# Performance work log

Measured on AMD Instinct MI355X. Metric: run time of the kernel, lower is better.

Reference implementation:

```python
import jax, jax.numpy as jnp
import numpy as np

D_MODEL = 1024
N_REG = 8
D_REG = 32
LN_EPS = 1e-5


def setup_inputs() -> dict:
    key = jax.random.key(0)
    ks = jax.random.split(key, 14)
    s = 0.02
    return {
        "x": jax.random.normal(ks[0], (8, 2048, D_MODEL), dtype=jnp.float32),
        "ln_w": jnp.ones((D_MODEL,), jnp.float32),
        "ln_b": jnp.zeros((D_MODEL,), jnp.float32),
        "Wrq": jax.random.normal(ks[1], (N_REG, D_MODEL), jnp.float32) * s,
        "brq": jax.random.normal(ks[2], (N_REG,), jnp.float32) * s,
        "Wrp": jax.random.normal(ks[3], (D_MODEL, D_REG), jnp.float32) * s,
        "brp": jax.random.normal(ks[4], (D_MODEL,), jnp.float32) * s,
        "Wwq": jax.random.normal(ks[5], (N_REG, D_MODEL), jnp.float32) * s,
        "bwq": jax.random.normal(ks[6], (N_REG,), jnp.float32) * s,
        "Wwv": jax.random.normal(ks[7], (D_REG, D_MODEL), jnp.float32) * s,
        "bwv": jax.random.normal(ks[8], (D_REG,), jnp.float32) * s,
        "Wwg": jax.random.normal(ks[9], (1, D_MODEL), jnp.float32) * s,
        "bwg": jnp.full((1,), -3.0, jnp.float32),
        "mix": jnp.asarray(0.001, jnp.float32),
    }


def _layernorm(x, w, b):
    mu = jnp.mean(x, axis=-1, keepdims=True)
    var = jnp.mean(jnp.square(x - mu), axis=-1, keepdims=True)
    return (x - mu) * jax.lax.rsqrt(var + LN_EPS) * w + b


def _forward(x, ln_w, ln_b, Wrq, brq, Wrp, brp, Wwq, bwq, Wwv, bwv, Wwg, bwg, mix):
    B, L, D = x.shape
    h = _layernorm(x, ln_w, ln_b)  # (B,L,D)
    # Precompute all per-timestep projections as big GEMMs (same math as per-step Linear)
    r_w = jax.nn.softmax(jnp.einsum("bld,rd->blr", h, Wrq) + brq, axis=-1)  # (B,L,R)
    w_w = jax.nn.softmax(jnp.einsum("bld,rd->blr", h, Wwq) + bwq, axis=-1)  # (B,L,R)
    w_v = jnp.einsum("bld,kd->blk", h, Wwv) + bwv                           # (B,L,Dr)
    w_g = jax.nn.sigmoid(jnp.einsum("bld,od->blo", h, Wwg) + bwg)           # (B,L,1)

    def step(registers, inputs):
        rw_t, ww_t, wv_t, wg_t = inputs  # (B,R), (B,R), (B,Dr), (B,1)
        r_v = jnp.einsum("br,brd->bd", rw_t, registers)  # read (B,Dr)
        us = (ww_t * wg_t)[..., None]                     # (B,R,1)
        new_regs = (1.0 - us) * registers + us * wv_t[:, None, :]
        return new_regs, r_v

    init_regs = jnp.zeros((B, N_REG, D_REG), x.dtype)
    seq = (
        jnp.moveaxis(r_w, 1, 0),
        jnp.moveaxis(w_w, 1, 0),
        jnp.moveaxis(w_v, 1, 0),
        jnp.moveaxis(w_g, 1, 0),
    )
    _, r_vs = jax.lax.scan(step, init_regs, seq)  # (L,B,Dr)
    r_vs = jnp.moveaxis(r_vs, 0, 1)               # (B,L,Dr)
    r_out = jnp.einsum("blk,dk->bld", r_vs, Wrp) + brp  # read_proj
    return mix * r_out


def reference(x, ln_w, ln_b, Wrq, brq, Wrp, brp, Wwq, bwq, Wwv, bwv, Wwg, bwg, mix):
    return _forward(x, ln_w, ln_b, Wrq, brq, Wrp, brp, Wwq, bwq, Wwv, bwv, Wwg, bwg, mix)
```

## Files before the change

### kernel.cpp

```cpp
#include <hip/hip_runtime.h>

#define D_MODEL 1024
#define L_SEQ   2048
#define N_BATCH 8
#define N_TOK   (N_BATCH * L_SEQ)
#define N_REGS  8
#define D_REG   32
#define N_CHUNK 64
#define CHUNK   32
#define LN_EPS  1e-5f

#define KC      32
#define XSTR    65
#define XQ      (KC * XSTR)
#define SSTR    57

__device__ __forceinline__ float wred(float v) {
    #pragma unroll
    for (int off = 32; off > 0; off >>= 1) v += __shfl_xor(v, off, 64);
    return v;
}

__device__ __forceinline__ float sigmoidf(float z) {
    return 1.f / (1.f + expf(-z));
}

__global__ __launch_bounds__(256) void k_prep(
    const float* __restrict__ ln_w, const float* __restrict__ ln_b,
    const float* __restrict__ Wrq,  const float* __restrict__ brq,
    const float* __restrict__ Wwq,  const float* __restrict__ bwq,
    const float* __restrict__ Wwv,  const float* __restrict__ bwv,
    const float* __restrict__ Wwg,  const float* __restrict__ bwg,
    float* __restrict__ Wpp, float* __restrict__ c1, float* __restrict__ c2)
{
    const int f = blockIdx.x;
    const int g = f / 13, i = f % 13;

    const float* wrow = nullptr; float bias = 0.f;
    if (f < 8)        { wrow = Wrq + f * D_MODEL;        bias = brq[f]; }
    else if (f < 16)  { wrow = Wwq + (f - 8) * D_MODEL;  bias = bwq[f - 8]; }
    else if (f == 16) { wrow = Wwg;                      bias = bwg[0]; }
    else if (f < 49)  { wrow = Wwv + (f - 17) * D_MODEL; bias = bwv[f - 17]; }

    float p1 = 0.f, p2 = 0.f;
    #pragma unroll
    for (int j = 0; j < 4; ++j) {
        const int k = j * 256 + threadIdx.x;
        float w  = wrow ? wrow[k] : 0.f;
        float wg = w * ln_w[k];
        Wpp[((size_t)(g * D_MODEL + k)) * 16 + i] = wg;
        p1 += wg;
        p2 = fmaf(w, ln_b[k], p2);
    }
    p1 = wred(p1); p2 = wred(p2);

    __shared__ float r1[4], r2[4];
    const int l = threadIdx.x & 63, w = threadIdx.x >> 6;
    if (l == 0) { r1[w] = p1; r2[w] = p2; }
    __syncthreads();
    if (threadIdx.x == 0) {
        c1[f] = r1[0] + r1[1] + r1[2] + r1[3];
        c2[f] = r2[0] + r2[1] + r2[2] + r2[3] + bias;
    }
}

template<int STATS>
__device__ __forceinline__ void proj_chunk(
    const float* __restrict__ lx,
    const float4* __restrict__ wr0,
    int lane, float acc[13], float& st)
{
    #pragma unroll 4
    for (int k = 0; k < KC; ++k) {
        const float xs = lx[k * XSTR + lane];
        const float4* wr = wr0 + (k << 2);
        float4 wa = wr[0], wb = wr[1], wc = wr[2];
        float  wd = reinterpret_cast<const float*>(wr)[12];
        acc[0]  = fmaf(xs, wa.x, acc[0]);
        acc[1]  = fmaf(xs, wa.y, acc[1]);
        acc[2]  = fmaf(xs, wa.z, acc[2]);
        acc[3]  = fmaf(xs, wa.w, acc[3]);
        acc[4]  = fmaf(xs, wb.x, acc[4]);
        acc[5]  = fmaf(xs, wb.y, acc[5]);
        acc[6]  = fmaf(xs, wb.z, acc[6]);
        acc[7]  = fmaf(xs, wb.w, acc[7]);
        acc[8]  = fmaf(xs, wc.x, acc[8]);
        acc[9]  = fmaf(xs, wc.y, acc[9]);
        acc[10] = fmaf(xs, wc.z, acc[10]);
        acc[11] = fmaf(xs, wc.w, acc[11]);
        acc[12] = fmaf(xs, wd,   acc[12]);
        if (STATS == 1) st += xs;
        if (STATS == 2) st = fmaf(xs, xs, st);
    }
}

__global__ __launch_bounds__(1024) void k_lnproj3(
    const float* __restrict__ x,
    const float* __restrict__ Wpp,
    const float* __restrict__ c1, const float* __restrict__ c2,
    float* __restrict__ rw_o, float* __restrict__ us_o, float* __restrict__ wv_o)
{
    extern __shared__ float lds[];
    float* Sb = lds + 2 * 4 * XQ;

    const int tid  = threadIdx.x;
    const int lane = tid & 63;
    const int wv   = tid >> 6;
    const int g    = wv & 3;
    const int kh   = wv >> 2;
    const int tok0 = blockIdx.x * 64;

    const int gs  = __builtin_amdgcn_readfirstlane(g);
    const int khs = __builtin_amdgcn_readfirstlane(kh);

    const int tq  = tid & 255;
    const int row = tq >> 3;
    const int c4  = tq & 7;

    const float4* x4 = reinterpret_cast<const float4*>(x);

    float4 xg[2];
    float acc[13];
    #pragma unroll
    for (int i = 0; i < 13; ++i) acc[i] = 0.f;
    float st = 0.f;

    const size_t gbase = (size_t)(tok0 + row) * 256 + khs * 64 + c4;

    {
        xg[0] = x4[gbase];
        xg[1] = x4[gbase + 32 * 256];
        float* dst = lds + khs * XQ + (c4 * 4) * XSTR;
        #pragma unroll
        for (int p = 0; p < 2; ++p) {
            const int r = row + 32 * p;
            dst[0 * XSTR + r] = xg[p].x;
            dst[1 * XSTR + r] = xg[p].y;
            dst[2 * XSTR + r] = xg[p].z;
            dst[3 * XSTR + r] = xg[p].w;
        }
    }
    __syncthreads();

    for (int c = 0; c < 8; ++c) {
        if (c < 7)  {
            xg[0] = x4[gbase + (size_t)(c + 1) * 8];
            xg[1] = x4[gbase + (size_t)(c + 1) * 8 + 32 * 256];
        }

        const float*  lx  = lds + ((c & 1) * 4 + khs) * XQ;
        const float4* wr0 = reinterpret_cast<const float4*>(Wpp)
                          + ((gs * D_MODEL + khs * 256 + c * KC) << 2);
        if (gs == 1)      proj_chunk<1>(lx, wr0, lane, acc, st);
        else if (gs == 2) proj_chunk<2>(lx, wr0, lane, acc, st);
        else              proj_chunk<0>(lx, wr0, lane, acc, st);

        if (c < 7) {
            float* dst = lds + (((c + 1) & 1) * 4 + khs) * XQ + (c4 * 4) * XSTR;
            #pragma unroll
            for (int p = 0; p < 2; ++p) {
                const int r = row + 32 * p;
                dst[0 * XSTR + r] = xg[p].x;
                dst[1 * XSTR + r] = xg[p].y;
                dst[2 * XSTR + r] = xg[p].z;
                dst[3 * XSTR + r] = xg[p].w;
            }
        }
        __syncthreads();
    }

    if (kh == 0) {
        #pragma unroll
        for (int i = 0; i < 13; ++i) Sb[lane * SSTR + g * 13 + i] = acc[i];
        if (g == 1) Sb[lane * SSTR + 52] = st;
        if (g == 2) Sb[lane * SSTR + 53] = st;
    }
    __syncthreads();
    #pragma unroll
    for (int ph = 1; ph < 4; ++ph) {
        if (kh == ph) {
            #pragma unroll
            for (int i = 0; i < 13; ++i) Sb[lane * SSTR + g * 13 + i] += acc[i];
            if (g == 1) Sb[lane * SSTR + 52] += st;
            if (g == 2) Sb[lane * SSTR + 53] += st;
        }
        __syncthreads();
    }

    if (tid < 256) {
        const int t  = tid & 63;
        const int q  = tid >> 6;
        const int tg = blockIdx.x * 64 + t;
        const float* St = Sb + t * SSTR;

        const float tsum = St[52], tss = St[53];
        const float mu  = tsum * (1.f / D_MODEL);
        const float var = tss * (1.f / D_MODEL) - mu * mu;
        const float rs  = rsqrtf(var + LN_EPS);

        if (q == 0) {
            float lg[8];
            #pragma unroll
            for (int r = 0; r < 8; ++r)
                lg[r] = rs * (St[r] - mu * c1[r]) + c2[r];
            float m = lg[0];
            #pragma unroll
            for (int r = 1; r < 8; ++r) m = fmaxf(m, lg[r]);
            float sm = 0.f;
            #pragma unroll
            for (int r = 0; r < 8; ++r) { lg[r] = expf(lg[r] - m); sm += lg[r]; }
            float inv = 1.f / sm;
            float4* o = reinterpret_cast<float4*>(rw_o + (size_t)tg * 8);
            o[0] = make_float4(lg[0]*inv, lg[1]*inv, lg[2]*inv, lg[3]*inv);
            o[1] = make_float4(lg[4]*inv, lg[5]*inv, lg[6]*inv, lg[7]*inv);
        } else if (q == 1) {
            float lg[8];
            #pragma unroll
            for (int r = 0; r < 8; ++r)
                lg[r] = rs * (St[8 + r] - mu * c1[8 + r]) + c2[8 + r];
            float gl = rs * (St[16] - mu * c1[16]) + c2[16];
            float m = lg[0];
            #pragma unroll
            for (int r = 1; r < 8; ++r) m = fmaxf(m, lg[r]);
            float sm = 0.f;
            #pragma unroll
            for (int r = 0; r < 8; ++r) { lg[r] = expf(lg[r] - m); sm += lg[r]; }
            float inv = sigmoidf(gl) / sm;
            float4* o = reinterpret_cast<float4*>(us_o + (size_t)tg * 8);
            o[0] = make_float4(lg[0]*inv, lg[1]*inv, lg[2]*inv, lg[3]*inv);
            o[1] = make_float4(lg[4]*inv, lg[5]*inv, lg[6]*inv, lg[7]*inv);
        } else {
            const int f0 = 17 + (q - 2) * 16;
            float4* o = reinterpret_cast<float4*>(wv_o + (size_t)tg * 32 + (q - 2) * 16);
            #pragma unroll
            for (int jq = 0; jq < 4; ++jq) {
                float v0 = rs * (St[f0 + jq*4 + 0] - mu * c1[f0 + jq*4 + 0]) + c2[f0 + jq*4 + 0];
                float v1 = rs * (St[f0 + jq*4 + 1] - mu * c1[f0 + jq*4 + 1]) + c2[f0 + jq*4 + 1];
                float v2 = rs * (St[f0 + jq*4 + 2] - mu * c1[f0 + jq*4 + 2]) + c2[f0 + jq*4 + 2];
                float v3 = rs * (St[f0 + jq*4 + 3] - mu * c1[f0 + jq*4 + 3]) + c2[f0 + jq*4 + 3];
                o[jq] = make_float4(v0, v1, v2, v3);
            }
        }
    }
}

__global__ __launch_bounds__(256) void k_chunk(
    const float* __restrict__ us, const float* __restrict__ wv,
    float* __restrict__ A, float* __restrict__ Bc)
{
    const int gid  = blockIdx.x * 256 + threadIdx.x;
    const int k    = gid & 31;
    const int unit = gid >> 5;
    const int ch   = unit & 63;
    const int br   = unit >> 6;
    const int b    = br >> 3, r = br & 7;
    const int t0   = ch * CHUNK;

    const float* usp = us + ((size_t)(b * L_SEQ + t0)) * 8 + r;
    const float* wvp = wv + ((size_t)(b * L_SEQ + t0)) * 32 + k;

    float Aacc = 1.f, Bacc = 0.f;
    #pragma unroll 4
    for (int t = 0; t < CHUNK; ++t) {
        float u = usp[t * 8];
        float w = wvp[t * 32];
        float a = 1.f - u;
        Aacc *= a;
        Bacc = a * Bacc + u * w;
    }
    Bc[(size_t)unit * 32 + k] = Bacc;
    if (k == 0) A[unit] = Aacc;
}

__global__ __launch_bounds__(64) void k_chain(
    const float* __restrict__ A, const float* __restrict__ Bc,
    float* __restrict__ S0)
{
    const int gid = blockIdx.x * 64 + threadIdx.x;
    const int k   = gid & 31;
    const int br  = gid >> 5;
    float st = 0.f;
    #pragma unroll 4
    for (int ch = 0; ch < N_CHUNK; ++ch) {
        const int unit = br * N_CHUNK + ch;
        S0[(size_t)unit * 32 + k] = st;
        st = A[unit] * st + Bc[(size_t)unit * 32 + k];
    }
}

__global__ __launch_bounds__(64) void k_replay(
    const float* __restrict__ rw, const float* __restrict__ us,
    const float* __restrict__ wv, const float* __restrict__ S0,
    float* __restrict__ rvs)
{
    const int gid  = blockIdx.x * 64 + threadIdx.x;
    const int k    = gid & 31;
    const int unit = gid >> 5;
    const int ch   = unit & 63;
    const int b    = unit >> 6;

    float s[8];
    #pragma unroll
    for (int r = 0; r < 8; ++r)
        s[r] = S0[((size_t)((b * 8 + r) * N_CHUNK) + ch) * 32 + k];

    const int t0 = b * L_SEQ + ch * CHUNK;
    const float* rwp = rw + (size_t)t0 * 8;
    const float* usp = us + (size_t)t0 * 8;
    const float* wvp = wv + (size_t)t0 * 32 + k;
    float*       rvp = rvs + (size_t)t0 * 32 + k;

    for (int t = 0; t < CHUNK; ++t) {
        float4 rw0 = reinterpret_cast<const float4*>(rwp + t * 8)[0];
        float4 rw1 = reinterpret_cast<const float4*>(rwp + t * 8)[1];
        float4 us0 = reinterpret_cast<const float4*>(usp + t * 8)[0];
        float4 us1 = reinterpret_cast<const float4*>(usp + t * 8)[1];
        float  w   = wvp[t * 32];

        float rv = rw0.x*s[0] + rw0.y*s[1] + rw0.z*s[2] + rw0.w*s[3]
                 + rw1.x*s[4] + rw1.y*s[5] + rw1.z*s[6] + rw1.w*s[7];
        rvp[t * 32] = rv;

        s[0] = (1.f - us0.x)*s[0] + us0.x*w;
        s[1] = (1.f - us0.y)*s[1] + us0.y*w;
        s[2] = (1.f - us0.z)*s[2] + us0.z*w;
        s[3] = (1.f - us0.w)*s[3] + us0.w*w;
        s[4] = (1.f - us1.x)*s[4] + us1.x*w;
        s[5] = (1.f - us1.y)*s[5] + us1.y*w;
        s[6] = (1.f - us1.z)*s[6] + us1.z*w;
        s[7] = (1.f - us1.w)*s[7] + us1.w*w;
    }
}

__global__ __launch_bounds__(256) void k_outproj(
    const float* __restrict__ rvs, const float* __restrict__ Wrp,
    const float* __restrict__ brp, const float* __restrict__ mix_p,
    float* __restrict__ out)
{
    const int d    = blockIdx.y * 256 + threadIdx.x;
    const int tok0 = blockIdx.x * 64;

    float4 wr[8];
    #pragma unroll
    for (int q = 0; q < 8; ++q)
        wr[q] = reinterpret_cast<const float4*>(Wrp)[(size_t)d * 8 + q];

    const float bias = brp[d];
    const float mix  = mix_p[0];

    for (int t = 0; t < 64; ++t) {
        const float4* rv = reinterpret_cast<const float4*>(rvs + (size_t)(tok0 + t) * 32);
        float acc = 0.f;
        #pragma unroll
        for (int q = 0; q < 8; ++q) {
            float4 v = rv[q];
            acc += wr[q].x*v.x + wr[q].y*v.y + wr[q].z*v.z + wr[q].w*v.w;
        }
        out[(size_t)(tok0 + t) * D_MODEL + d] = mix * (acc + bias);
    }
}

extern "C" void kernel_launch(void* const* d_in, const int* in_sizes, int n_in,
                              void* d_out, int out_size, void* d_ws, size_t ws_size,
                              hipStream_t stream)
{
    const float* x    = (const float*)d_in[0];
    const float* ln_w = (const float*)d_in[1];
    const float* ln_b = (const float*)d_in[2];
    const float* Wrq  = (const float*)d_in[3];
    const float* brq  = (const float*)d_in[4];
    const float* Wrp  = (const float*)d_in[5];
    const float* brp  = (const float*)d_in[6];
    const float* Wwq  = (const float*)d_in[7];
    const float* bwq  = (const float*)d_in[8];
    const float* Wwv  = (const float*)d_in[9];
    const float* bwv  = (const float*)d_in[10];
    const float* Wwg  = (const float*)d_in[11];
    const float* bwg  = (const float*)d_in[12];
    const float* mix  = (const float*)d_in[13];
    float* out = (float*)d_out;

    float* ws   = (float*)d_ws;
    float* rw_b = ws;
    float* us_b = ws + 131072;
    float* wv_b = ws + 262144;
    float* A_b  = ws + 786432;
    float* B_b  = ws + 790528;
    float* S0_b = ws + 921600;
    float* rv_b = ws + 1052672;
    float* Wpp  = rv_b;
    float* c1_b = rv_b + 65536;
    float* c2_b = rv_b + 65600;

    const size_t lds_bytes = (size_t)(2 * 4 * XQ + 64 * SSTR) * 4;

    k_prep<<<52, 256, 0, stream>>>(ln_w, ln_b, Wrq, brq, Wwq, bwq,
                                   Wwv, bwv, Wwg, bwg, Wpp, c1_b, c2_b);
    k_lnproj3<<<256, 1024, lds_bytes, stream>>>(x, Wpp, c1_b, c2_b,
                                                rw_b, us_b, wv_b);
    k_chunk <<<512, 256, 0, stream>>>(us_b, wv_b, A_b, B_b);
    k_chain <<<32,  64,  0, stream>>>(A_b, B_b, S0_b);
    k_replay<<<256, 64,  0, stream>>>(rw_b, us_b, wv_b, S0_b, rv_b);
    dim3 gc(N_TOK / 64, 4);
    k_outproj<<<gc, 256, 0, stream>>>(rv_b, Wrp, brp, mix, out);
}
```

Baseline: 94.99 us.

## Fuse chunk summary and chain scan into one kernel, shorten replay chunks

Merges the chunk-summary and chain kernels into a single k_scan kernel. Each block handles one (batch, register) pair, stages the update weights in LDS and runs the cross-chunk carry in shared memory, which removes one launch and the global round trip for the A/B summaries. Chunks shrink from 32 to 16 steps, so the replay kernel has more independent units and shorter serial chains, and it now batches its loads per group of four steps and uses fma updates. The output projection computes four output columns per thread with float4 stores. The costs are a serial 128-step chain run by one wavefront per block, only 64 scan blocks, and much higher register pressure in outproj from holding 128 weight floats per thread.

New measurement: 105.2 us. 1.11x slower.

```diff
diff --git a/kernel.cpp b/kernel.cpp
--- a/kernel.cpp
+++ b/kernel.cpp
@@ -6,14 +6,15 @@
 #define N_TOK   (N_BATCH * L_SEQ)
 #define N_REGS  8
 #define D_REG   32
-#define N_CHUNK 64
-#define CHUNK   32
 #define LN_EPS  1e-5f
 
 #define KC      32
 #define XSTR    65
 #define XQ      (KC * XSTR)
 #define SSTR    57
+
+#define HSTEP   16
+#define N_HALF  128
 
 __device__ __forceinline__ float wred(float v) {
     #pragma unroll
@@ -244,119 +245,153 @@
     }
 }
 
-__global__ __launch_bounds__(256) void k_chunk(
+__global__ __launch_bounds__(1024) void k_scan(
     const float* __restrict__ us, const float* __restrict__ wv,
-    float* __restrict__ A, float* __restrict__ Bc)
-{
-    const int gid  = blockIdx.x * 256 + threadIdx.x;
-    const int k    = gid & 31;
-    const int unit = gid >> 5;
-    const int ch   = unit & 63;
-    const int br   = unit >> 6;
-    const int b    = br >> 3, r = br & 7;
-    const int t0   = ch * CHUNK;
-
-    const float* usp = us + ((size_t)(b * L_SEQ + t0)) * 8 + r;
-    const float* wvp = wv + ((size_t)(b * L_SEQ + t0)) * 32 + k;
-
-    float Aacc = 1.f, Bacc = 0.f;
-    #pragma unroll 4
-    for (int t = 0; t < CHUNK; ++t) {
-        float u = usp[t * 8];
-        float w = wvp[t * 32];
-        float a = 1.f - u;
-        Aacc *= a;
-        Bacc = a * Bacc + u * w;
-    }
-    Bc[(size_t)unit * 32 + k] = Bacc;
-    if (k == 0) A[unit] = Aacc;
-}
-
-__global__ __launch_bounds__(64) void k_chain(
-    const float* __restrict__ A, const float* __restrict__ Bc,
     float* __restrict__ S0)
 {
-    const int gid = blockIdx.x * 64 + threadIdx.x;
-    const int k   = gid & 31;
-    const int br  = gid >> 5;
-    float st = 0.f;
-    #pragma unroll 4
-    for (int ch = 0; ch < N_CHUNK; ++ch) {
-        const int unit = br * N_CHUNK + ch;
-        S0[(size_t)unit * 32 + k] = st;
-        st = A[unit] * st + Bc[(size_t)unit * 32 + k];
-    }
-}
-
-__global__ __launch_bounds__(64) void k_replay(
+    __shared__ float S_us[L_SEQ];
+    __shared__ float lA[N_HALF];
+    __shared__ float lB[N_HALF * 32];
+
+    const int tid = threadIdx.x;
+    const int b   = blockIdx.x >> 3;
+    const int r   = blockIdx.x & 7;
+
+    #pragma unroll
+    for (int i = 0; i < 2; ++i) {
+        const int t = i * 1024 + tid;
+        S_us[t] = us[((size_t)(b * L_SEQ + t)) * 8 + r];
+    }
+    __syncthreads();
+
+    const int k  = tid & 31;
+    const int hb = (tid >> 5) * 4;
+    #pragma unroll
+    for (int j = 0; j < 4; ++j) {
+        const int h  = hb + j;
+        const int t0 = h * HSTEP;
+        const float* wvp = wv + ((size_t)(b * L_SEQ + t0)) * 32 + k;
+
+        float Aacc = 1.f, Bacc = 0.f;
+        #pragma unroll
+        for (int gq = 0; gq < 2; ++gq) {
+            float wl[8], ul[8];
+            #pragma unroll
+            for (int e = 0; e < 8; ++e) {
+                wl[e] = wvp[(gq * 8 + e) * 32];
+                ul[e] = S_us[t0 + gq * 8 + e];
+            }
+            #pragma unroll
+            for (int e = 0; e < 8; ++e) {
+                float a = 1.f - ul[e];
+                Aacc *= a;
+                Bacc = fmaf(a, Bacc, ul[e] * wl[e]);
+            }
+        }
+        lB[h * 32 + k] = Bacc;
+        if (k == 0) lA[h] = Aacc;
+    }
+    __syncthreads();
+
+    if (tid < 32) {
+        float stv = 0.f;
+        float* S0p = S0 + ((size_t)(b * 8 + r) * N_HALF) * 32 + tid;
+        for (int h = 0; h < N_HALF; ++h) {
+            S0p[h * 32] = stv;
+            stv = fmaf(lA[h], stv, lB[h * 32 + tid]);
+        }
+    }
+}
+
+__global__ __launch_bounds__(256) void k_replay2(
     const float* __restrict__ rw, const float* __restrict__ us,
     const float* __restrict__ wv, const float* __restrict__ S0,
     float* __restrict__ rvs)
 {
-    const int gid  = blockIdx.x * 64 + threadIdx.x;
-    const int k    = gid & 31;
-    const int unit = gid >> 5;
-    const int ch   = unit & 63;
-    const int b    = unit >> 6;
+    const int gid = blockIdx.x * 256 + threadIdx.x;
+    const int k   = gid & 31;
+    const int hu  = gid >> 5;
+    const int b   = hu >> 7;
+    const int ch2 = hu & 127;
 
     float s[8];
     #pragma unroll
     for (int r = 0; r < 8; ++r)
-        s[r] = S0[((size_t)((b * 8 + r) * N_CHUNK) + ch) * 32 + k];
-
-    const int t0 = b * L_SEQ + ch * CHUNK;
+        s[r] = S0[((size_t)((b * 8 + r) * N_HALF) + ch2) * 32 + k];
+
+    const int t0 = b * L_SEQ + ch2 * HSTEP;
     const float* rwp = rw + (size_t)t0 * 8;
     const float* usp = us + (size_t)t0 * 8;
     const float* wvp = wv + (size_t)t0 * 32 + k;
     float*       rvp = rvs + (size_t)t0 * 32 + k;
 
-    for (int t = 0; t < CHUNK; ++t) {
-        float4 rw0 = reinterpret_cast<const float4*>(rwp + t * 8)[0];
-        float4 rw1 = reinterpret_cast<const float4*>(rwp + t * 8)[1];
-        float4 us0 = reinterpret_cast<const float4*>(usp + t * 8)[0];
-        float4 us1 = reinterpret_cast<const float4*>(usp + t * 8)[1];
-        float  w   = wvp[t * 32];
-
-        float rv = rw0.x*s[0] + rw0.y*s[1] + rw0.z*s[2] + rw0.w*s[3]
-                 + rw1.x*s[4] + rw1.y*s[5] + rw1.z*s[6] + rw1.w*s[7];
-        rvp[t * 32] = rv;
-
-        s[0] = (1.f - us0.x)*s[0] + us0.x*w;
-        s[1] = (1.f - us0.y)*s[1] + us0.y*w;
-        s[2] = (1.f - us0.z)*s[2] + us0.z*w;
-        s[3] = (1.f - us0.w)*s[3] + us0.w*w;
-        s[4] = (1.f - us1.x)*s[4] + us1.x*w;
-        s[5] = (1.f - us1.y)*s[5] + us1.y*w;
-        s[6] = (1.f - us1.z)*s[6] + us1.z*w;
-        s[7] = (1.f - us1.w)*s[7] + us1.w*w;
-    }
-}
-
-__global__ __launch_bounds__(256) void k_outproj(
+    #pragma unroll
+    for (int g4 = 0; g4 < 4; ++g4) {
+        float4 r0[4], r1[4], u0[4], u1[4];
+        float  wl[4];
+        #pragma unroll
+        for (int j = 0; j < 4; ++j) {
+            const int t = g4 * 4 + j;
+            r0[j] = reinterpret_cast<const float4*>(rwp + t * 8)[0];
+            r1[j] = reinterpret_cast<const float4*>(rwp + t * 8)[1];
+            u0[j] = reinterpret_cast<const float4*>(usp + t * 8)[0];
+            u1[j] = reinterpret_cast<const float4*>(usp + t * 8)[1];
+            wl[j] = wvp[t * 32];
+        }
+        #pragma unroll
+        for (int j = 0; j < 4; ++j) {
+            const int t = g4 * 4 + j;
+            float rv = r0[j].x*s[0] + r0[j].y*s[1] + r0[j].z*s[2] + r0[j].w*s[3]
+                     + r1[j].x*s[4] + r1[j].y*s[5] + r1[j].z*s[6] + r1[j].w*s[7];
+            rvp[t * 32] = rv;
+            const float w = wl[j];
+            s[0] = fmaf(u0[j].x, w - s[0], s[0]);
+            s[1] = fmaf(u0[j].y, w - s[1], s[1]);
+            s[2] = fmaf(u0[j].z, w - s[2], s[2]);
+            s[3] = fmaf(u0[j].w, w - s[3], s[3]);
+            s[4] = fmaf(u1[j].x, w - s[4], s[4]);
+            s[5] = fmaf(u1[j].y, w - s[5], s[5]);
+            s[6] = fmaf(u1[j].z, w - s[6], s[6]);
+            s[7] = fmaf(u1[j].w, w - s[7], s[7]);
+        }
+    }
+}
+
+__global__ __launch_bounds__(256) void k_outproj2(
     const float* __restrict__ rvs, const float* __restrict__ Wrp,
     const float* __restrict__ brp, const float* __restrict__ mix_p,
     float* __restrict__ out)
 {
-    const int d    = blockIdx.y * 256 + threadIdx.x;
+    const int d0   = threadIdx.x * 4;
     const int tok0 = blockIdx.x * 64;
 
-    float4 wr[8];
-    #pragma unroll
-    for (int q = 0; q < 8; ++q)
-        wr[q] = reinterpret_cast<const float4*>(Wrp)[(size_t)d * 8 + q];
-
-    const float bias = brp[d];
-    const float mix  = mix_p[0];
+    float4 wr[4][8];
+    #pragma unroll
+    for (int i = 0; i < 4; ++i)
+        #pragma unroll
+        for (int q = 0; q < 8; ++q)
+            wr[i][q] = reinterpret_cast<const float4*>(Wrp)[(size_t)(d0 + i) * 8 + q];
+
+    const float4 bias = *reinterpret_cast<const float4*>(brp + d0);
+    const float  mix  = mix_p[0];
 
     for (int t = 0; t < 64; ++t) {
         const float4* rv = reinterpret_cast<const float4*>(rvs + (size_t)(tok0 + t) * 32);
-        float acc = 0.f;
-        #pragma unroll
-        for (int q = 0; q < 8; ++q) {
-            float4 v = rv[q];
-            acc += wr[q].x*v.x + wr[q].y*v.y + wr[q].z*v.z + wr[q].w*v.w;
-        }
-        out[(size_t)(tok0 + t) * D_MODEL + d] = mix * (acc + bias);
+        float4 v[8];
+        #pragma unroll
+        for (int q = 0; q < 8; ++q) v[q] = rv[q];
+
+        float acc[4] = {0.f, 0.f, 0.f, 0.f};
+        #pragma unroll
+        for (int i = 0; i < 4; ++i)
+            #pragma unroll
+            for (int q = 0; q < 8; ++q)
+                acc[i] += wr[i][q].x*v[q].x + wr[i][q].y*v[q].y
+                        + wr[i][q].z*v[q].z + wr[i][q].w*v[q].w;
+
+        float4 o = make_float4(mix * (acc[0] + bias.x), mix * (acc[1] + bias.y),
+                               mix * (acc[2] + bias.z), mix * (acc[3] + bias.w));
+        *reinterpret_cast<float4*>(out + (size_t)(tok0 + t) * D_MODEL + d0) = o;
     }
 }
 
@@ -384,10 +419,8 @@
     float* rw_b = ws;
     float* us_b = ws + 131072;
     float* wv_b = ws + 262144;
-    float* A_b  = ws + 786432;
-    float* B_b  = ws + 790528;
-    float* S0_b = ws + 921600;
-    float* rv_b = ws + 1052672;
+    float* S0_b = ws + 786432;
+    float* rv_b = ws + 1048576;
     float* Wpp  = rv_b;
     float* c1_b = rv_b + 65536;
     float* c2_b = rv_b + 65600;
@@ -398,9 +431,7 @@
                                    Wwv, bwv, Wwg, bwg, Wpp, c1_b, c2_b);
     k_lnproj3<<<256, 1024, lds_bytes, stream>>>(x, Wpp, c1_b, c2_b,
                                                 rw_b, us_b, wv_b);
-    k_chunk <<<512, 256, 0, stream>>>(us_b, wv_b, A_b, B_b);
-    k_chain <<<32,  64,  0, stream>>>(A_b, B_b, S0_b);
-    k_replay<<<256, 64,  0, stream>>>(rw_b, us_b, wv_b, S0_b, rv_b);
-    dim3 gc(N_TOK / 64, 4);
-    k_outproj<<<gc, 256, 0, stream>>>(rv_b, Wrp, brp, mix, out);
-}
+    k_scan   <<<64, 1024, 0, stream>>>(us_b, wv_b, S0_b);
+    k_replay2<<<128, 256, 0, stream>>>(rw_b, us_b, wv_b, S0_b, rv_b);
+    k_outproj2<<<256, 256, 0, stream>>>(rv_b, Wrp, brp, mix, out);
+}
```
